# Optimization experiments

Measured on AMD Instinct MI355X. Metric: run time of the kernel, lower is better.

Reference implementation:

```python
import jax, jax.numpy as jnp
import numpy as np

DIM_IN = 512
HIDDEN = 512
DIM_OUT = 512
BATCH = 256

def _n_tri(d):
    return (d * d + d) // 2

def _quad_expand(x):
    # x: [B, D] -> [B, D + (D^2+D)/2] with upper-triu (incl diag) pairwise products
    d = x.shape[1]
    iu0, iu1 = np.triu_indices(d)  # static indices
    x_sq = x[:, iu0] * x[:, iu1]  # [B, n_tri] -- avoids materializing full outer
    return jnp.concatenate([x, x_sq], axis=-1)

def setup_inputs() -> dict:
    key = jax.random.key(0)
    k = jax.random.split(key, 5)
    f0 = DIM_IN + _n_tri(DIM_IN)
    f1 = HIDDEN + _n_tri(HIDDEN)
    s0 = 1.0 / np.sqrt(f0)
    s1 = 1.0 / np.sqrt(f1)
    return {
        "x": jax.random.normal(k[0], (BATCH, DIM_IN), dtype=jnp.float32),
        "W0": jax.random.uniform(k[1], (HIDDEN, f0), dtype=jnp.float32, minval=-s0, maxval=s0),
        "b0": jax.random.uniform(k[2], (HIDDEN,), dtype=jnp.float32, minval=-s0, maxval=s0),
        "W1": jax.random.uniform(k[3], (DIM_OUT, f1), dtype=jnp.float32, minval=-s1, maxval=s1),
        "b1": jax.random.uniform(k[4], (DIM_OUT,), dtype=jnp.float32, minval=-s1, maxval=s1),
    }

def reference(x, W0, b0, W1, b1):
    h = _quad_expand(x) @ W0.T + b0  # [B, HIDDEN]
    out = _quad_expand(h) @ W1.T + b1  # [B, DIM_OUT]
    return out
```

## Files before the change

### kernel.cpp

```cpp
#include <hip/hip_runtime.h>

typedef short s16x8 __attribute__((ext_vector_type(8)));
typedef float f32x4 __attribute__((ext_vector_type(4)));

#define DIM     512
#define BATCH   256
#define NTRI    131328
#define FDIM    131840
#define KBLOCKS 2060
#define BN      64
#define NTILES  8
#define CCH     64

__device__ __forceinline__ unsigned short f2bf(float f) {
  __bf16 h = (__bf16)f;
  return __builtin_bit_cast(unsigned short, h);
}
__device__ __forceinline__ float bf2f(unsigned short s) {
  union { unsigned u; float f; } v; v.u = (unsigned)s << 16; return v.f;
}
__device__ __forceinline__ unsigned pk2(float a, float b) {
  return (unsigned)f2bf(a) | ((unsigned)f2bf(b) << 16);
}
__device__ __forceinline__ int swz(int m) { return (m ^ (m >> 2)) & 7; }

__device__ __forceinline__ void dma16(const void* g, void* l) {
  __builtin_amdgcn_global_load_lds(
      (const __attribute__((address_space(1))) void*)g,
      (__attribute__((address_space(3))) void*)l, 16, 0, 0);
}

__global__ void setup(unsigned* __restrict__ table, const float* __restrict__ x,
                      unsigned short* __restrict__ Xt) {
  int bid = blockIdx.x;
  if (bid < 512) {
    int i = bid;
    int base = i * DIM - (i * (i - 1)) / 2;
    int len = DIM - i;
    for (int t = threadIdx.x; t < len; t += blockDim.x)
      table[base + t] = ((unsigned)i << 16) | (unsigned)(i + t);
  } else {
    int t = (bid - 512) * blockDim.x + threadIdx.x;
    int r = t & (BATCH - 1);
    int c = t >> 8;
    Xt[c * BATCH + r] = f2bf(x[r * DIM + c]);
  }
}

__global__ __launch_bounds__(512)
void featgen(const unsigned* __restrict__ table,
             const unsigned short* __restrict__ Xt,
             uint4* __restrict__ Feat)
{
  __shared__ uint4 img[2048];
  const int kb = blockIdx.x;
  const int tid = threadIdx.x;
  const int s8 = tid >> 6;
  const int lane = tid & 63;
  const int f0 = kb * 64 + s8 * 8;

  if (f0 < DIM) {
    #pragma unroll
    for (int mb = 0; mb < 4; ++mb) {
      int m = mb * 64 + lane;
      unsigned short v[8];
      #pragma unroll
      for (int e = 0; e < 8; ++e) v[e] = Xt[(f0 + e) * BATCH + m];
      uint4 pk;
      pk.x = (unsigned)v[0] | ((unsigned)v[1] << 16);
      pk.y = (unsigned)v[2] | ((unsigned)v[3] << 16);
      pk.z = (unsigned)v[4] | ((unsigned)v[5] << 16);
      pk.w = (unsigned)v[6] | ((unsigned)v[7] << 16);
      img[m * 8 + (s8 ^ swz(m))] = pk;
    }
  } else {
    int p0 = f0 - DIM;
    unsigned t0 = table[p0], t7 = table[p0 + 7];
    if ((t0 >> 16) == (t7 >> 16)) {
      int i = (int)(t0 >> 16), j0 = (int)(t0 & 0xffffu);
      #pragma unroll
      for (int mb = 0; mb < 4; ++mb) {
        int m = mb * 64 + lane;
        float xi = bf2f(Xt[i * BATCH + m]);
        float pr[8];
        #pragma unroll
        for (int e = 0; e < 8; ++e) pr[e] = xi * bf2f(Xt[(j0 + e) * BATCH + m]);
        uint4 pk = make_uint4(pk2(pr[0], pr[1]), pk2(pr[2], pr[3]),
                              pk2(pr[4], pr[5]), pk2(pr[6], pr[7]));
        img[m * 8 + (s8 ^ swz(m))] = pk;
      }
    } else {
      unsigned tt[8];
      #pragma unroll
      for (int e = 0; e < 8; ++e) tt[e] = table[p0 + e];
      #pragma unroll
      for (int mb = 0; mb < 4; ++mb) {
        int m = mb * 64 + lane;
        float pr[8];
        #pragma unroll
        for (int e = 0; e < 8; ++e)
          pr[e] = bf2f(Xt[(tt[e] >> 16) * BATCH + m]) * bf2f(Xt[(tt[e] & 0xffffu) * BATCH + m]);
        uint4 pk = make_uint4(pk2(pr[0], pr[1]), pk2(pr[2], pr[3]),
                              pk2(pr[4], pr[5]), pk2(pr[6], pr[7]));
        img[m * 8 + (s8 ^ swz(m))] = pk;
      }
    }
  }
  __syncthreads();
  uint4* out = Feat + (size_t)kb * 2048;
  #pragma unroll
  for (int p = 0; p < 4; ++p) out[p * 512 + tid] = img[p * 512 + tid];
}

__global__ __launch_bounds__(512, 4)
void qgemm(const uint4* __restrict__ Feat,
           const float* __restrict__ W,
           unsigned short* __restrict__ partial,
           int C)
{
  __shared__ unsigned short As[2 * BATCH * 64];
  __shared__ unsigned short Ws[2 * 64 * 64];
  const int chunk = blockIdx.x % C;
  const int ntile = blockIdx.x / C;
  const int kb0 = (KBLOCKS * chunk) / C;
  const int kb1 = (KBLOCKS * (chunk + 1)) / C;
  const int n0 = ntile * BN;
  const int tid = threadIdx.x;
  const int lane = tid & 63;
  const int wave = tid >> 6;
  const int wm = wave & 3;
  const int wn = wave >> 2;
  const int lm = lane & 15;
  const int lk = lane >> 4;

  const int wr0 = tid >> 4;
  const int wc16 = tid & 15;

  f32x4 acc[4][2] = {};
  f32x4 wregC[2], wregN[2];

  const char* fsrc0 = (const char*)Feat + tid * 16;
  char* adst0 = (char*)As + tid * 16;
  const float* wp0 = W + (size_t)(n0 + wr0) * FDIM + wc16 * 4;
  const size_t wrow32 = (size_t)32 * FDIM;

  {
    const char* src = fsrc0 + (size_t)kb0 * 32768;
    #pragma unroll
    for (int p = 0; p < 4; ++p) dma16(src + p * 8192, adst0 + p * 8192);
    #pragma unroll
    for (int it = 0; it < 2; ++it)
      wregC[it] = *(const f32x4*)(wp0 + it * wrow32 + (size_t)kb0 * 64);
  }

  for (int kb = kb0; kb < kb1 - 1; ++kb) {
    const int pc = (kb - kb0) & 1;
    {
      const char* src = fsrc0 + (size_t)(kb + 1) * 32768;
      char* dst = adst0 + (pc ^ 1) * 32768;
      #pragma unroll
      for (int p = 0; p < 4; ++p) dma16(src + p * 8192, dst + p * 8192);
      #pragma unroll
      for (int it = 0; it < 2; ++it)
        wregN[it] = *(const f32x4*)(wp0 + it * wrow32 + (size_t)(kb + 1) * 64);
    }
    __builtin_amdgcn_sched_barrier(0);
    #pragma unroll
    for (int it = 0; it < 2; ++it) {
      int r = wr0 + it * 32;
      int slot = (wc16 >> 1) ^ swz(r);
      *(uint2*)((char*)Ws + pc * 8192 + r * 128 + slot * 16 + (wc16 & 1) * 8) =
          make_uint2(pk2(wregC[it][0], wregC[it][1]), pk2(wregC[it][2], wregC[it][3]));
    }
    asm volatile("s_waitcnt lgkmcnt(0)" ::: "memory");
    __builtin_amdgcn_sched_barrier(0);
    __builtin_amdgcn_s_barrier();
    {
      const char* asb = (const char*)As + pc * 32768;
      const char* wsb = (const char*)Ws + pc * 8192;
      s16x8 bfr[2][2], afr[2][4];
      #pragma unroll
      for (int ks = 0; ks < 2; ++ks) {
        #pragma unroll
        for (int nf = 0; nf < 2; ++nf) {
          int n = wn * 32 + nf * 16 + lm;
          int slot = (ks * 4 + lk) ^ swz(n);
          bfr[ks][nf] = *(const s16x8*)(wsb + n * 128 + slot * 16);
        }
        #pragma unroll
        for (int mf = 0; mf < 4; ++mf) {
          int mm = wm * 64 + mf * 16 + lm;
          int slot = (ks * 4 + lk) ^ swz(mm);
          afr[ks][mf] = *(const s16x8*)(asb + mm * 128 + slot * 16);
        }
      }
      __builtin_amdgcn_s_setprio(1);
      #pragma unroll
      for (int ks = 0; ks < 2; ++ks)
        #pragma unroll
        for (int mf = 0; mf < 4; ++mf)
          #pragma unroll
          for (int nf = 0; nf < 2; ++nf)
            acc[mf][nf] = __builtin_amdgcn_mfma_f32_16x16x32_bf16(afr[ks][mf], bfr[ks][nf], acc[mf][nf], 0, 0, 0);
      __builtin_amdgcn_s_setprio(0);
    }
    __builtin_amdgcn_s_barrier();
    wregC[0] = wregN[0]; wregC[1] = wregN[1];
  }

  {
    const int pc = (kb1 - 1 - kb0) & 1;
    #pragma unroll
    for (int it = 0; it < 2; ++it) {
      int r = wr0 + it * 32;
      int slot = (wc16 >> 1) ^ swz(r);
      *(uint2*)((char*)Ws + pc * 8192 + r * 128 + slot * 16 + (wc16 & 1) * 8) =
          make_uint2(pk2(wregC[it][0], wregC[it][1]), pk2(wregC[it][2], wregC[it][3]));
    }
    asm volatile("s_waitcnt lgkmcnt(0)" ::: "memory");
    __builtin_amdgcn_s_barrier();
    const char* asb = (const char*)As + pc * 32768;
    const char* wsb = (const char*)Ws + pc * 8192;
    s16x8 bfr[2][2], afr[2][4];
    #pragma unroll
    for (int ks = 0; ks < 2; ++ks) {
      #pragma unroll
      for (int nf = 0; nf < 2; ++nf) {
        int n = wn * 32 + nf * 16 + lm;
        int slot = (ks * 4 + lk) ^ swz(n);
        bfr[ks][nf] = *(const s16x8*)(wsb + n * 128 + slot * 16);
      }
      #pragma unroll
      for (int mf = 0; mf < 4; ++mf) {
        int mm = wm * 64 + mf * 16 + lm;
        int slot = (ks * 4 + lk) ^ swz(mm);
        afr[ks][mf] = *(const s16x8*)(asb + mm * 128 + slot * 16);
      }
    }
    #pragma unroll
    for (int ks = 0; ks < 2; ++ks)
      #pragma unroll
      for (int mf = 0; mf < 4; ++mf)
        #pragma unroll
        for (int nf = 0; nf < 2; ++nf)
          acc[mf][nf] = __builtin_amdgcn_mfma_f32_16x16x32_bf16(afr[ks][mf], bfr[ks][nf], acc[mf][nf], 0, 0, 0);
  }

  unsigned short* pout = partial + (size_t)chunk * (BATCH * DIM);
  #pragma unroll
  for (int mf = 0; mf < 4; ++mf) {
    #pragma unroll
    for (int nf = 0; nf < 2; ++nf) {
      int mrow = wm * 64 + mf * 16 + lk * 4;
      int ncol = n0 + wn * 32 + nf * 16 + lm;
      #pragma unroll
      for (int r = 0; r < 4; ++r)
        pout[(size_t)(mrow + r) * DIM + ncol] = f2bf(acc[mf][nf][r]);
    }
  }
}

__global__ void reduce_h(const unsigned short* __restrict__ partial, const float* __restrict__ bias,
                         unsigned short* __restrict__ Ht, int C) {
  int u = blockIdx.x * blockDim.x + threadIdx.x;
  int t8 = u * 8;
  int b = t8 >> 9;
  int o0 = t8 & (DIM - 1);
  float s[8];
  #pragma unroll
  for (int e = 0; e < 8; ++e) s[e] = bias[o0 + e];
  for (int c = 0; c < C; ++c) {
    uint4 v = *(const uint4*)(partial + (size_t)c * (BATCH * DIM) + t8);
    unsigned w[4] = {v.x, v.y, v.z, v.w};
    #pragma unroll
    for (int p = 0; p < 4; ++p) {
      s[2*p]   += bf2f((unsigned short)(w[p] & 0xffffu));
      s[2*p+1] += bf2f((unsigned short)(w[p] >> 16));
    }
  }
  #pragma unroll
  for (int e = 0; e < 8; ++e)
    Ht[(o0 + e) * BATCH + b] = f2bf(s[e]);
}

__global__ void reduce_out(const unsigned short* __restrict__ partial, const float* __restrict__ bias,
                           float* __restrict__ out, int C) {
  int u = blockIdx.x * blockDim.x + threadIdx.x;
  int t8 = u * 8;
  int o0 = t8 & (DIM - 1);
  float s[8];
  #pragma unroll
  for (int e = 0; e < 8; ++e) s[e] = bias[o0 + e];
  for (int c = 0; c < C; ++c) {
    uint4 v = *(const uint4*)(partial + (size_t)c * (BATCH * DIM) + t8);
    unsigned w[4] = {v.x, v.y, v.z, v.w};
    #pragma unroll
    for (int p = 0; p < 4; ++p) {
      s[2*p]   += bf2f((unsigned short)(w[p] & 0xffffu));
      s[2*p+1] += bf2f((unsigned short)(w[p] >> 16));
    }
  }
  f32x4 lo = {s[0], s[1], s[2], s[3]};
  f32x4 hi = {s[4], s[5], s[6], s[7]};
  *(f32x4*)(out + t8) = lo;
  *(f32x4*)(out + t8 + 4) = hi;
}

extern "C" void kernel_launch(void* const* d_in, const int* in_sizes, int n_in,
                              void* d_out, int out_size, void* d_ws, size_t ws_size,
                              hipStream_t stream) {
  const float* x  = (const float*)d_in[0];
  const float* W0 = (const float*)d_in[1];
  const float* b0 = (const float*)d_in[2];
  const float* W1 = (const float*)d_in[3];
  const float* b1 = (const float*)d_in[4];
  float* out = (float*)d_out;

  char* ws = (char*)d_ws;
  unsigned* table    = (unsigned*)ws;
  unsigned short* Xt = (unsigned short*)(ws + 525312);
  unsigned short* Ht = (unsigned short*)(ws + 787456);
  uint4* Feat        = (uint4*)(ws + 1049600);
  size_t feat_end    = 1049600 + (size_t)KBLOCKS * 32768;
  unsigned short* partial = (unsigned short*)(ws + feat_end);

  size_t avail = (ws_size > feat_end) ? (ws_size - feat_end) : 0;
  int C = (int)(avail / ((size_t)BATCH * DIM * sizeof(unsigned short)));
  if (C > CCH) C = CCH;
  if (C < 1)  C = 1;

  setup<<<dim3(1024), dim3(256), 0, stream>>>(table, x, Xt);

  featgen<<<dim3(KBLOCKS), dim3(512), 0, stream>>>(table, Xt, Feat);
  qgemm<<<dim3(NTILES * C), dim3(512), 0, stream>>>(Feat, W0, partial, C);
  reduce_h<<<dim3(64), dim3(256), 0, stream>>>(partial, b0, Ht, C);

  featgen<<<dim3(KBLOCKS), dim3(512), 0, stream>>>(table, Ht, Feat);
  qgemm<<<dim3(NTILES * C), dim3(512), 0, stream>>>(Feat, W1, partial, C);
  reduce_out<<<dim3(64), dim3(256), 0, stream>>>(partial, b1, out, C);
}
```

Baseline: 238.3 us.

## Load feature fragments directly into registers, dropping LDS staging for activations

```diff
diff --git a/kernel.cpp b/kernel.cpp
--- a/kernel.cpp
+++ b/kernel.cpp
@@ -23,12 +23,6 @@
   return (unsigned)f2bf(a) | ((unsigned)f2bf(b) << 16);
 }
 __device__ __forceinline__ int swz(int m) { return (m ^ (m >> 2)) & 7; }
-
-__device__ __forceinline__ void dma16(const void* g, void* l) {
-  __builtin_amdgcn_global_load_lds(
-      (const __attribute__((address_space(1))) void*)g,
-      (__attribute__((address_space(3))) void*)l, 16, 0, 0);
-}
 
 __global__ void setup(unsigned* __restrict__ table, const float* __restrict__ x,
                       unsigned short* __restrict__ Xt) {
@@ -52,12 +46,12 @@
              const unsigned short* __restrict__ Xt,
              uint4* __restrict__ Feat)
 {
-  __shared__ uint4 img[2048];
   const int kb = blockIdx.x;
   const int tid = threadIdx.x;
   const int s8 = tid >> 6;
   const int lane = tid & 63;
   const int f0 = kb * 64 + s8 * 8;
+  uint4* out = Feat + ((size_t)kb * 8 + s8) * 256;
 
   if (f0 < DIM) {
     #pragma unroll
@@ -71,7 +65,7 @@
       pk.y = (unsigned)v[2] | ((unsigned)v[3] << 16);
       pk.z = (unsigned)v[4] | ((unsigned)v[5] << 16);
       pk.w = (unsigned)v[6] | ((unsigned)v[7] << 16);
-      img[m * 8 + (s8 ^ swz(m))] = pk;
+      out[m] = pk;
     }
   } else {
     int p0 = f0 - DIM;
@@ -85,9 +79,8 @@
         float pr[8];
         #pragma unroll
         for (int e = 0; e < 8; ++e) pr[e] = xi * bf2f(Xt[(j0 + e) * BATCH + m]);
-        uint4 pk = make_uint4(pk2(pr[0], pr[1]), pk2(pr[2], pr[3]),
-                              pk2(pr[4], pr[5]), pk2(pr[6], pr[7]));
-        img[m * 8 + (s8 ^ swz(m))] = pk;
+        out[m] = make_uint4(pk2(pr[0], pr[1]), pk2(pr[2], pr[3]),
+                            pk2(pr[4], pr[5]), pk2(pr[6], pr[7]));
       }
     } else {
       unsigned tt[8];
@@ -100,16 +93,11 @@
         #pragma unroll
         for (int e = 0; e < 8; ++e)
           pr[e] = bf2f(Xt[(tt[e] >> 16) * BATCH + m]) * bf2f(Xt[(tt[e] & 0xffffu) * BATCH + m]);
-        uint4 pk = make_uint4(pk2(pr[0], pr[1]), pk2(pr[2], pr[3]),
-                              pk2(pr[4], pr[5]), pk2(pr[6], pr[7]));
-        img[m * 8 + (s8 ^ swz(m))] = pk;
+        out[m] = make_uint4(pk2(pr[0], pr[1]), pk2(pr[2], pr[3]),
+                            pk2(pr[4], pr[5]), pk2(pr[6], pr[7]));
       }
     }
   }
-  __syncthreads();
-  uint4* out = Feat + (size_t)kb * 2048;
-  #pragma unroll
-  for (int p = 0; p < 4; ++p) out[p * 512 + tid] = img[p * 512 + tid];
 }
 
 __global__ __launch_bounds__(512, 4)
@@ -118,8 +106,7 @@
            unsigned short* __restrict__ partial,
            int C)
 {
-  __shared__ unsigned short As[2 * BATCH * 64];
-  __shared__ unsigned short Ws[2 * 64 * 64];
+  __shared__ unsigned short Ws[2][4096];
   const int chunk = blockIdx.x % C;
   const int ntile = blockIdx.x / C;
   const int kb0 = (KBLOCKS * chunk) / C;
@@ -128,131 +115,93 @@
   const int tid = threadIdx.x;
   const int lane = tid & 63;
   const int wave = tid >> 6;
-  const int wm = wave & 3;
-  const int wn = wave >> 2;
   const int lm = lane & 15;
   const int lk = lane >> 4;
 
   const int wr0 = tid >> 4;
   const int wc16 = tid & 15;
 
-  f32x4 acc[4][2] = {};
-  f32x4 wregC[2], wregN[2];
-
-  const char* fsrc0 = (const char*)Feat + tid * 16;
-  char* adst0 = (char*)As + tid * 16;
+  f32x4 acc[2][4] = {};
+  f32x4 wregC[2], wregN[2], wT[2];
+  uint4 afrC[2][2], afrN[2][2];
+
   const float* wp0 = W + (size_t)(n0 + wr0) * FDIM + wc16 * 4;
   const size_t wrow32 = (size_t)32 * FDIM;
-
-  {
-    const char* src = fsrc0 + (size_t)kb0 * 32768;
-    #pragma unroll
-    for (int p = 0; p < 4; ++p) dma16(src + p * 8192, adst0 + p * 8192);
+  const int abase = lk * 256 + wave * 32 + lm;
+
+  auto loadA = [&](uint4 (*a)[2], int kb) {
+    #pragma unroll
+    for (int mf = 0; mf < 2; ++mf)
+      #pragma unroll
+      for (int ks = 0; ks < 2; ++ks)
+        a[mf][ks] = Feat[(size_t)kb * 2048 + ks * 1024 + mf * 16 + abase];
+  };
+  auto loadWr = [&](f32x4* w, int kb) {
     #pragma unroll
     for (int it = 0; it < 2; ++it)
-      wregC[it] = *(const f32x4*)(wp0 + it * wrow32 + (size_t)kb0 * 64);
-  }
-
-  for (int kb = kb0; kb < kb1 - 1; ++kb) {
-    const int pc = (kb - kb0) & 1;
-    {
-      const char* src = fsrc0 + (size_t)(kb + 1) * 32768;
-      char* dst = adst0 + (pc ^ 1) * 32768;
-      #pragma unroll
-      for (int p = 0; p < 4; ++p) dma16(src + p * 8192, dst + p * 8192);
-      #pragma unroll
-      for (int it = 0; it < 2; ++it)
-        wregN[it] = *(const f32x4*)(wp0 + it * wrow32 + (size_t)(kb + 1) * 64);
-    }
-    __builtin_amdgcn_sched_barrier(0);
+      w[it] = *(const f32x4*)(wp0 + it * wrow32 + (size_t)kb * 64);
+  };
+  auto storeWs = [&](int buf, const f32x4* w) {
     #pragma unroll
     for (int it = 0; it < 2; ++it) {
       int r = wr0 + it * 32;
       int slot = (wc16 >> 1) ^ swz(r);
-      *(uint2*)((char*)Ws + pc * 8192 + r * 128 + slot * 16 + (wc16 & 1) * 8) =
-          make_uint2(pk2(wregC[it][0], wregC[it][1]), pk2(wregC[it][2], wregC[it][3]));
-    }
-    asm volatile("s_waitcnt lgkmcnt(0)" ::: "memory");
-    __builtin_amdgcn_sched_barrier(0);
-    __builtin_amdgcn_s_barrier();
-    {
-      const char* asb = (const char*)As + pc * 32768;
-      const char* wsb = (const char*)Ws + pc * 8192;
-      s16x8 bfr[2][2], afr[2][4];
-      #pragma unroll
-      for (int ks = 0; ks < 2; ++ks) {
-        #pragma unroll
-        for (int nf = 0; nf < 2; ++nf) {
-          int n = wn * 32 + nf * 16 + lm;
-          int slot = (ks * 4 + lk) ^ swz(n);
-          bfr[ks][nf] = *(const s16x8*)(wsb + n * 128 + slot * 16);
-        }
-        #pragma unroll
-        for (int mf = 0; mf < 4; ++mf) {
-          int mm = wm * 64 + mf * 16 + lm;
-          int slot = (ks * 4 + lk) ^ swz(mm);
-          afr[ks][mf] = *(const s16x8*)(asb + mm * 128 + slot * 16);
-        }
+      *(uint2*)((char*)&Ws[buf][0] + r * 128 + slot * 16 + (wc16 & 1) * 8) =
+          make_uint2(pk2(w[it][0], w[it][1]), pk2(w[it][2], w[it][3]));
+    }
+  };
+  auto compute = [&](int buf, uint4 (*a)[2]) {
+    #pragma unroll
+    for (int ks = 0; ks < 2; ++ks) {
+      s16x8 bfr[4];
+      #pragma unroll
+      for (int nf = 0; nf < 4; ++nf) {
+        int n = nf * 16 + lm;
+        int slot = (ks * 4 + lk) ^ swz(n);
+        bfr[nf] = *(const s16x8*)((const char*)&Ws[buf][0] + n * 128 + slot * 16);
       }
       __builtin_amdgcn_s_setprio(1);
       #pragma unroll
-      for (int ks = 0; ks < 2; ++ks)
+      for (int mf = 0; mf < 2; ++mf)
         #pragma unroll
-        for (int mf = 0; mf < 4; ++mf)
-          #pragma unroll
-          for (int nf = 0; nf < 2; ++nf)
-            acc[mf][nf] = __builtin_amdgcn_mfma_f32_16x16x32_bf16(afr[ks][mf], bfr[ks][nf], acc[mf][nf], 0, 0, 0);
+        for (int nf = 0; nf < 4; ++nf)
+          acc[mf][nf] = __builtin_amdgcn_mfma_f32_16x16x32_bf16(
+              __builtin_bit_cast(s16x8, a[mf][ks]), bfr[nf], acc[mf][nf], 0, 0, 0);
       __builtin_amdgcn_s_setprio(0);
     }
-    __builtin_amdgcn_s_barrier();
-    wregC[0] = wregN[0]; wregC[1] = wregN[1];
-  }
-
-  {
-    const int pc = (kb1 - 1 - kb0) & 1;
-    #pragma unroll
-    for (int it = 0; it < 2; ++it) {
-      int r = wr0 + it * 32;
-      int slot = (wc16 >> 1) ^ swz(r);
-      *(uint2*)((char*)Ws + pc * 8192 + r * 128 + slot * 16 + (wc16 & 1) * 8) =
-          make_uint2(pk2(wregC[it][0], wregC[it][1]), pk2(wregC[it][2], wregC[it][3]));
-    }
+  };
+
+  loadA(afrC, kb0);
+  loadWr(wT, kb0);
+  loadWr(wregC, min(kb0 + 1, KBLOCKS - 1));
+  storeWs(kb0 & 1, wT);
+  asm volatile("s_waitcnt lgkmcnt(0)" ::: "memory");
+  __builtin_amdgcn_s_barrier();
+
+  for (int kb = kb0; kb < kb1 - 1; ++kb) {
+    const int buf = kb & 1;
+    loadA(afrN, kb + 1);
+    loadWr(wregN, min(kb + 2, KBLOCKS - 1));
+    storeWs(buf ^ 1, wregC);
+    compute(buf, afrC);
     asm volatile("s_waitcnt lgkmcnt(0)" ::: "memory");
     __builtin_amdgcn_s_barrier();
-    const char* asb = (const char*)As + pc * 32768;
-    const char* wsb = (const char*)Ws + pc * 8192;
-    s16x8 bfr[2][2], afr[2][4];
-    #pragma unroll
-    for (int ks = 0; ks < 2; ++ks) {
-      #pragma unroll
-      for (int nf = 0; nf < 2; ++nf) {
-        int n = wn * 32 + nf * 16 + lm;
-        int slot = (ks * 4 + lk) ^ swz(n);
-        bfr[ks][nf] = *(const s16x8*)(wsb + n * 128 + slot * 16);
-      }
-      #pragma unroll
-      for (int mf = 0; mf < 4; ++mf) {
-        int mm = wm * 64 + mf * 16 + lm;
-        int slot = (ks * 4 + lk) ^ swz(mm);
-        afr[ks][mf] = *(const s16x8*)(asb + mm * 128 + slot * 16);
-      }
-    }
-    #pragma unroll
-    for (int ks = 0; ks < 2; ++ks)
-      #pragma unroll
-      for (int mf = 0; mf < 4; ++mf)
-        #pragma unroll
-        for (int nf = 0; nf < 2; ++nf)
-          acc[mf][nf] = __builtin_amdgcn_mfma_f32_16x16x32_bf16(afr[ks][mf], bfr[ks][nf], acc[mf][nf], 0, 0, 0);
-  }
+    #pragma unroll
+    for (int mf = 0; mf < 2; ++mf) {
+      afrC[mf][0] = afrN[mf][0]; afrC[mf][1] = afrN[mf][1];
+    }
+    wregC[0] = wregN[0]; wregC[1] = wregN[1];
+  }
+
+  compute((kb1 - 1) & 1, afrC);
 
   unsigned short* pout = partial + (size_t)chunk * (BATCH * DIM);
   #pragma unroll
-  for (int mf = 0; mf < 4; ++mf) {
-    #pragma unroll
-    for (int nf = 0; nf < 2; ++nf) {
-      int mrow = wm * 64 + mf * 16 + lk * 4;
-      int ncol = n0 + wn * 32 + nf * 16 + lm;
+  for (int mf = 0; mf < 2; ++mf) {
+    #pragma unroll
+    for (int nf = 0; nf < 4; ++nf) {
+      int mrow = wave * 32 + mf * 16 + lk * 4;
+      int ncol = n0 + nf * 16 + lm;
       #pragma unroll
       for (int r = 0; r < 4; ++r)
         pout[(size_t)(mrow + r) * DIM + ncol] = f2bf(acc[mf][nf][r]);
```

Measured after the change: 243.5 us. 1.02x slower.
